# Kernel optimization log

Measured on AMD Instinct MI355X. Metric: run time of the kernel, lower is better.

## Reference

```python
import jax, jax.numpy as jnp
import numpy as np

NEG_SLOPE = 0.2
STRONG_CONVEXITY = 0.5


def _scalar(x, Wq, Wl, bl, Wz, wz_out, wq_out, wl_out):
    # x: [B, D]; Wq/Wl: [L, H, D]; bl: [L, H]; Wz: [L-1, H, H]
    # Precompute all per-layer x-dependent terms in two batched einsums.
    qx = jnp.einsum('lhd,bd->lbh', Wq, x) ** 2          # [L, B, H]
    lx = jnp.einsum('lhd,bd->lbh', Wl, x) + bl[:, None, :]  # [L, B, H]
    z = jax.nn.leaky_relu(qx[0] + lx[0], negative_slope=NEG_SLOPE)

    def step(z, inputs):
        W, q, l = inputs
        z = jax.nn.leaky_relu(z @ W.T + q + l, negative_slope=NEG_SLOPE)
        return z, None

    z, _ = jax.lax.scan(step, z, (Wz, qx[1:], lx[1:]))
    # Final layer to scalar output (no bias on last wx_lin per torch code).
    out = z @ wz_out.T + (x @ wq_out.T) ** 2 + x @ wl_out.T  # [B, 1]
    return out


def setup_inputs() -> dict:
    key = jax.random.key(0)
    ks = jax.random.split(key, 8)
    B, D, H, L = 8192, 128, 512, 10
    f32 = jnp.float32
    x = jax.random.normal(ks[0], (B, D), f32)
    Wq = jax.random.normal(ks[1], (L, H, D), f32) * (1.0 / np.sqrt(D))
    Wl = jax.random.normal(ks[2], (L, H, D), f32) * (1.0 / np.sqrt(D))
    bl = jax.random.normal(ks[3], (L, H), f32) * 0.01
    # wz weights are kept non-negative in the original (clamp/exp init)
    Wz = jnp.abs(jax.random.normal(ks[4], (L - 1, H, H), f32)) * (1.0 / np.sqrt(H))
    wz_out = jnp.abs(jax.random.normal(ks[5], (1, H), f32)) * (1.0 / np.sqrt(H))
    wq_out = jax.random.normal(ks[6], (1, D), f32) * (1.0 / np.sqrt(D))
    wl_out = jax.random.normal(ks[7], (1, D), f32) * (1.0 / np.sqrt(D))
    return {"x": x, "Wq": Wq, "Wl": Wl, "bl": bl, "Wz": Wz,
            "wz_out": wz_out, "wq_out": wq_out, "wl_out": wl_out}


def reference(x, Wq, Wl, bl, Wz, wz_out, wq_out, wl_out):
    # forward = (1 - mu) * d(scalar)/dx + mu * x, with grad_outputs = ones
    def scalar_sum(xx):
        return jnp.sum(_scalar(xx, Wq, Wl, bl, Wz, wz_out, wq_out, wl_out))

    gx = jax.grad(scalar_sum)(x)  # per-sample gradient, [B, D]
    return (1.0 - STRONG_CONVEXITY) * gx + STRONG_CONVEXITY * x
```

## Files before the change

### kernel.cpp

```cpp
#include <hip/hip_runtime.h>


#define Bn 8192
#define Dn 128
#define Hn 512
#define Ln 10

constexpr float NS = 0.2f;

typedef __attribute__((ext_vector_type(8))) short short8;
typedef __attribute__((ext_vector_type(4))) float f32x4;

typedef const __attribute__((address_space(1))) void GV;
typedef __attribute__((address_space(3))) void LV;

__device__ __forceinline__ void gload16(const void* g, void* l) {
    __builtin_amdgcn_global_load_lds((GV*)g, (LV*)l, 16, 0, 0);
}

#define MFMA(acc, a, b) acc = __builtin_amdgcn_mfma_f32_16x16x32_bf16(a, b, acc, 0, 0, 0)

__device__ __forceinline__ unsigned short bf16_rne(float v) {
    unsigned u = __float_as_uint(v);
    u += 0x7FFFu + ((u >> 16) & 1u);
    return (unsigned short)(u >> 16);
}
__device__ __forceinline__ float bf2f(unsigned short h) {
    return __uint_as_float(((unsigned)h) << 16);
}
__device__ __forceinline__ void split2(float v, unsigned short& h, unsigned short& l) {
    h = bf16_rne(v);
    l = bf16_rne(v - bf2f(h));
}


__global__ __launch_bounds__(256) void split_flat(const float* __restrict__ in,
        unsigned short* __restrict__ hi, unsigned short* __restrict__ lo, int n4) {
    int i = blockIdx.x * 256 + threadIdx.x;
    if (i >= n4) return;
    float4 v = ((const float4*)in)[i];
    ushort4 h, l;
    split2(v.x, h.x, l.x);
    split2(v.y, h.y, l.y);
    split2(v.z, h.z, l.z);
    split2(v.w, h.w, l.w);
    ((ushort4*)hi)[i] = h;
    ((ushort4*)lo)[i] = l;
}

__global__ __launch_bounds__(256) void split_both(const float* __restrict__ in,
        unsigned short* __restrict__ hi, unsigned short* __restrict__ lo,
        unsigned short* __restrict__ thi, unsigned short* __restrict__ tlo,
        int R, int C) {
    __shared__ float t[32][33];
    const size_t off = (size_t)blockIdx.z * R * C;
    const float* src = in + off;
    unsigned short* sh_ = hi + off;
    unsigned short* sl_ = lo + off;
    unsigned short* dh = thi + off;
    unsigned short* dl = tlo + off;
    const int r0 = blockIdx.x * 32, c0 = blockIdx.y * 32;
    const int tr = threadIdx.x >> 5, tc = threadIdx.x & 31;
#pragma unroll
    for (int i = 0; i < 4; ++i) {
        size_t si = (size_t)(r0 + tr + 8 * i) * C + c0 + tc;
        float v = src[si];
        t[tr + 8 * i][tc] = v;
        unsigned short h, l; split2(v, h, l);
        sh_[si] = h; sl_[si] = l;
    }
    __syncthreads();
#pragma unroll
    for (int i = 0; i < 4; ++i) {
        float v = t[tc][tr + 8 * i];
        unsigned short h, l; split2(v, h, l);
        size_t o = (size_t)(c0 + tr + 8 * i) * R + r0 + tc;
        dh[o] = h; dl[o] = l;
    }
}


__global__ __launch_bounds__(256) void fwd_mfma(
    const unsigned short* __restrict__ xh, const unsigned short* __restrict__ xl,
    const unsigned short* __restrict__ zph, const unsigned short* __restrict__ zpl,
    const unsigned short* __restrict__ Wzh, const unsigned short* __restrict__ Wzl,
    const unsigned short* __restrict__ Wqh, const unsigned short* __restrict__ Wql,
    const unsigned short* __restrict__ Wlh, const unsigned short* __restrict__ Wll,
    const float* __restrict__ bl,
    unsigned short* __restrict__ zoh, unsigned short* __restrict__ zol,
    unsigned short* __restrict__ mask16,
    unsigned short* __restrict__ uoh, unsigned short* __restrict__ uol, int hasZ)
{
    __shared__ __align__(16) char smem[32768];
    unsigned short* Ah  = (unsigned short*)smem;
    unsigned short* Al  = (unsigned short*)(smem + 8192);
    unsigned short* B0h = (unsigned short*)(smem + 16384);
    unsigned short* B0l = (unsigned short*)(smem + 20480);
    unsigned short* B1h = (unsigned short*)(smem + 24576);
    unsigned short* B1l = (unsigned short*)(smem + 28672);

    const int tid = threadIdx.x;
    const int w = tid >> 6, lane = tid & 63;
    const int lq = lane >> 4, lc = lane & 15;
    const int wm = (w & 1) * 64, wn = (w >> 1) * 32;
    const int row0 = blockIdx.x * 128, col0 = blockIdx.y * 64;
    const int sr = lane >> 2, sk = (lane & 3) * 8;

    f32x4 accz[4][2], accu[4][2], accv[4][2];
#pragma unroll
    for (int i = 0; i < 4; ++i)
#pragma unroll
        for (int j = 0; j < 2; ++j)
#pragma unroll
            for (int r = 0; r < 4; ++r) { accz[i][j][r] = 0.f; accu[i][j][r] = 0.f; accv[i][j][r] = 0.f; }

    if (hasZ) {
        for (int k0 = 0; k0 < Hn; k0 += 32) {
            __syncthreads();
            for (int c = w; c < 8; c += 4) {
                size_t go = (size_t)(row0 + c * 16 + sr) * Hn + k0 + sk;
                gload16(zph + go, Ah + c * 512);
                gload16(zpl + go, Al + c * 512);
            }
            {
                int c = w;
                size_t go = (size_t)(col0 + c * 16 + sr) * Hn + k0 + sk;
                gload16(Wzh + go, B0h + c * 512);
                gload16(Wzl + go, B0l + c * 512);
            }
            __syncthreads();
            short8 ah[4], al[4];
#pragma unroll
            for (int mt = 0; mt < 4; ++mt) {
                int ao = (wm + mt * 16 + lc) * 32 + lq * 8;
                ah[mt] = *(const short8*)(Ah + ao);
                al[mt] = *(const short8*)(Al + ao);
            }
#pragma unroll
            for (int nt = 0; nt < 2; ++nt) {
                int bo = (wn + nt * 16 + lc) * 32 + lq * 8;
                short8 bh = *(const short8*)(B0h + bo);
                short8 bv = *(const short8*)(B0l + bo);
#pragma unroll
                for (int mt = 0; mt < 4; ++mt) {
                    MFMA(accz[mt][nt], ah[mt], bh);
                    MFMA(accz[mt][nt], ah[mt], bv);
                    MFMA(accz[mt][nt], al[mt], bh);
                }
            }
        }
    }

    for (int k0 = 0; k0 < Dn; k0 += 32) {
        __syncthreads();
        for (int c = w; c < 8; c += 4) {
            size_t go = (size_t)(row0 + c * 16 + sr) * Dn + k0 + sk;
            gload16(xh + go, Ah + c * 512);
            gload16(xl + go, Al + c * 512);
        }
        {
            int c = w;
            size_t go = (size_t)(col0 + c * 16 + sr) * Dn + k0 + sk;
            gload16(Wqh + go, B0h + c * 512);
            gload16(Wql + go, B0l + c * 512);
            gload16(Wlh + go, B1h + c * 512);
            gload16(Wll + go, B1l + c * 512);
        }
        __syncthreads();
        short8 ah[4], al[4];
#pragma unroll
        for (int mt = 0; mt < 4; ++mt) {
            int ao = (wm + mt * 16 + lc) * 32 + lq * 8;
            ah[mt] = *(const short8*)(Ah + ao);
            al[mt] = *(const short8*)(Al + ao);
        }
#pragma unroll
        for (int nt = 0; nt < 2; ++nt) {
            int bo = (wn + nt * 16 + lc) * 32 + lq * 8;
            short8 bqh = *(const short8*)(B0h + bo);
            short8 bql = *(const short8*)(B0l + bo);
            short8 blh = *(const short8*)(B1h + bo);
            short8 bll = *(const short8*)(B1l + bo);
#pragma unroll
            for (int mt = 0; mt < 4; ++mt) {
                MFMA(accu[mt][nt], ah[mt], bqh);
                MFMA(accu[mt][nt], ah[mt], bql);
                MFMA(accu[mt][nt], al[mt], bqh);
                MFMA(accv[mt][nt], ah[mt], blh);
                MFMA(accv[mt][nt], ah[mt], bll);
                MFMA(accv[mt][nt], al[mt], blh);
            }
        }
    }

#pragma unroll
    for (int nt = 0; nt < 2; ++nt) {
        const int colb = col0 + wn + nt * 16;
        const int col = colb + lc;
        const float blv = bl[col];
#pragma unroll
        for (int mt = 0; mt < 4; ++mt) {
            const int rowb = row0 + wm + mt * 16;
#pragma unroll
            for (int r = 0; r < 4; ++r) {
                float uq = accu[mt][nt][r];
                float pre = accz[mt][nt][r] + uq * uq + accv[mt][nt][r] + blv;
                bool m = pre >= 0.f;
                unsigned long long bal = __ballot(m);
                if (lc == 0) {
                    int rw = rowb + lq * 4 + r;
                    mask16[(size_t)rw * 32 + (colb >> 4)] =
                        (unsigned short)((bal >> (lq * 16)) & 0xFFFFull);
                }
                float zv = m ? pre : NS * pre;
                unsigned short h, l; split2(zv, h, l);
                size_t o = (size_t)(rowb + lq * 4 + r) * Hn + col;
                zoh[o] = h; zol[o] = l;
                unsigned short uhh, ull; split2(uq, uhh, ull);
                uoh[o] = uhh; uol[o] = ull;
            }
        }
    }
}


__global__ __launch_bounds__(256) void bwd_combo(
    const unsigned short* __restrict__ gah, const unsigned short* __restrict__ gal,
    const unsigned short* __restrict__ WzTh, const unsigned short* __restrict__ WzTl,
    const unsigned short* __restrict__ maskprev,
    unsigned short* __restrict__ goh, unsigned short* __restrict__ gol,
    unsigned short* uph, unsigned short* upl,
    const unsigned short* __restrict__ a1h_, const unsigned short* __restrict__ a1l_,
    const unsigned short* __restrict__ WqTh, const unsigned short* __restrict__ WqTl,
    const unsigned short* __restrict__ WlTh, const unsigned short* __restrict__ WlTl,
    float* __restrict__ gx, int addTo, int nG, int finalF,
    const float* __restrict__ xin, const float* __restrict__ s,
    const float* __restrict__ wq_out, const float* __restrict__ wl_out)
{
    __shared__ __align__(16) char smem[24576];
    const int bid = blockIdx.x;
    const int tid = threadIdx.x;
    const int w = tid >> 6, lane = tid & 63;
    const int lq = lane >> 4, lc = lane & 15;
    const int sr = lane >> 2, sk = (lane & 3) * 8;

    if (bid < nG) {
        unsigned short* Ah  = (unsigned short*)smem;
        unsigned short* Al  = (unsigned short*)(smem + 8192);
        unsigned short* B0h = (unsigned short*)(smem + 16384);
        unsigned short* B0l = (unsigned short*)(smem + 20480);
        const int wm = (w & 1) * 64, wn = (w >> 1) * 32;
        const int row0 = (bid & 63) * 128, col0 = (bid >> 6) * 64;

        f32x4 acc[4][2];
#pragma unroll
        for (int i = 0; i < 4; ++i)
#pragma unroll
            for (int j = 0; j < 2; ++j)
#pragma unroll
                for (int r = 0; r < 4; ++r) acc[i][j][r] = 0.f;

        for (int k0 = 0; k0 < Hn; k0 += 32) {
            __syncthreads();
            for (int c = w; c < 8; c += 4) {
                size_t go = (size_t)(row0 + c * 16 + sr) * Hn + k0 + sk;
                gload16(gah + go, Ah + c * 512);
                gload16(gal + go, Al + c * 512);
            }
            {
                int c = w;
                size_t go = (size_t)(col0 + c * 16 + sr) * Hn + k0 + sk;
                gload16(WzTh + go, B0h + c * 512);
                gload16(WzTl + go, B0l + c * 512);
            }
            __syncthreads();
            short8 ah[4], al[4];
#pragma unroll
            for (int mt = 0; mt < 4; ++mt) {
                int ao = (wm + mt * 16 + lc) * 32 + lq * 8;
                ah[mt] = *(const short8*)(Ah + ao);
                al[mt] = *(const short8*)(Al + ao);
            }
#pragma unroll
            for (int nt = 0; nt < 2; ++nt) {
                int bo = (wn + nt * 16 + lc) * 32 + lq * 8;
                short8 bh = *(const short8*)(B0h + bo);
                short8 bv = *(const short8*)(B0l + bo);
#pragma unroll
                for (int mt = 0; mt < 4; ++mt) {
                    MFMA(acc[mt][nt], ah[mt], bh);
                    MFMA(acc[mt][nt], ah[mt], bv);
                    MFMA(acc[mt][nt], al[mt], bh);
                }
            }
        }

#pragma unroll
        for (int nt = 0; nt < 2; ++nt) {
            const int colb = col0 + wn + nt * 16;
            const int col = colb + lc;
#pragma unroll
            for (int mt = 0; mt < 4; ++mt) {
                const int rowb = row0 + wm + mt * 16;
#pragma unroll
                for (int r = 0; r < 4; ++r) {
                    int row = rowb + lq * 4 + r;
                    unsigned short wbits = maskprev[(size_t)row * 32 + (colb >> 4)];
                    float f = ((wbits >> lc) & 1) ? 1.f : NS;
                    float v = acc[mt][nt][r] * f;
                    unsigned short h, l; split2(v, h, l);
                    size_t o = (size_t)row * Hn + col;
                    goh[o] = h; gol[o] = l;
                    float uv = bf2f(uph[o]) + bf2f(upl[o]);
                    float a1v = 2.f * uv * v;
                    unsigned short h2, l2; split2(a1v, h2, l2);
                    uph[o] = h2; upl[o] = l2;
                }
            }
        }
    } else {
        unsigned short* Ah = (unsigned short*)smem;
        unsigned short* Al = (unsigned short*)(smem + 4096);
        unsigned short* Bh = (unsigned short*)(smem + 8192);
        unsigned short* Bl = (unsigned short*)(smem + 12288);
        const int wm = (w & 1) * 32, wn = (w >> 1) * 32;
        const int t = bid - nG;
        const int row0 = (t >> 1) * 64, col0 = (t & 1) * 64;

        f32x4 acc[2][2];
#pragma unroll
        for (int i = 0; i < 2; ++i)
#pragma unroll
            for (int j = 0; j < 2; ++j)
#pragma unroll
                for (int r = 0; r < 4; ++r) acc[i][j][r] = 0.f;

#pragma unroll
        for (int pass = 0; pass < 2; ++pass) {
            const unsigned short* Ash = pass ? gah : a1h_;
            const unsigned short* Asl = pass ? gal : a1l_;
            const unsigned short* Bsh = pass ? WlTh : WqTh;
            const unsigned short* Bsl = pass ? WlTl : WqTl;
            for (int k0 = 0; k0 < Hn; k0 += 32) {
                __syncthreads();
                {
                    int c = w;
                    size_t ga_ = (size_t)(row0 + c * 16 + sr) * Hn + k0 + sk;
                    gload16(Ash + ga_, Ah + c * 512);
                    gload16(Asl + ga_, Al + c * 512);
                    size_t gb_ = (size_t)(col0 + c * 16 + sr) * Hn + k0 + sk;
                    gload16(Bsh + gb_, Bh + c * 512);
                    gload16(Bsl + gb_, Bl + c * 512);
                }
                __syncthreads();
                short8 ah[2], al[2];
#pragma unroll
                for (int mt = 0; mt < 2; ++mt) {
                    int ao = (wm + mt * 16 + lc) * 32 + lq * 8;
                    ah[mt] = *(const short8*)(Ah + ao);
                    al[mt] = *(const short8*)(Al + ao);
                }
#pragma unroll
                for (int nt = 0; nt < 2; ++nt) {
                    int bo = (wn + nt * 16 + lc) * 32 + lq * 8;
                    short8 bh = *(const short8*)(Bh + bo);
                    short8 bv = *(const short8*)(Bl + bo);
#pragma unroll
                    for (int mt = 0; mt < 2; ++mt) {
                        MFMA(acc[mt][nt], ah[mt], bh);
                        MFMA(acc[mt][nt], ah[mt], bv);
                        MFMA(acc[mt][nt], al[mt], bh);
                    }
                }
            }
        }

#pragma unroll
        for (int nt = 0; nt < 2; ++nt) {
            const int col = col0 + wn + nt * 16 + lc;
#pragma unroll
            for (int mt = 0; mt < 2; ++mt) {
                const int rowb = row0 + wm + mt * 16;
#pragma unroll
                for (int r = 0; r < 4; ++r) {
                    const int row = rowb + lq * 4 + r;
                    size_t o = (size_t)row * Dn + col;
                    float v = acc[mt][nt][r];
                    if (addTo) v += gx[o];
                    if (finalF) {
                        v = 0.5f * v + s[row] * wq_out[col] + 0.5f * wl_out[col]
                            + 0.5f * xin[o];
                    }
                    gx[o] = v;
                }
            }
        }
    }
}


__global__ __launch_bounds__(256) void ga_init(
    const float* __restrict__ wz_out, const unsigned short* __restrict__ mask9,
    unsigned short* uh, unsigned short* ul,
    unsigned short* __restrict__ gh, unsigned short* __restrict__ gl)
{
    int i = blockIdx.x * 256 + threadIdx.x;
    int e = i << 2;
    int b = e >> 9, h = e & 511;
    unsigned short wbits = mask9[(size_t)b * 32 + (h >> 4)];
    float4 wv = *(const float4*)(wz_out + h);
    ushort4 u4h = *(const ushort4*)(uh + e);
    ushort4 u4l = *(const ushort4*)(ul + e);
    int sh = h & 15;
    ushort4 oh, ol, qh, ql;
    float f, a;
    f = wv.x * (((wbits >> (sh + 0)) & 1) ? 1.f : NS); split2(f, oh.x, ol.x);
    a = 2.f * (bf2f(u4h.x) + bf2f(u4l.x)) * f; split2(a, qh.x, ql.x);
    f = wv.y * (((wbits >> (sh + 1)) & 1) ? 1.f : NS); split2(f, oh.y, ol.y);
    a = 2.f * (bf2f(u4h.y) + bf2f(u4l.y)) * f; split2(a, qh.y, ql.y);
    f = wv.z * (((wbits >> (sh + 2)) & 1) ? 1.f : NS); split2(f, oh.z, ol.z);
    a = 2.f * (bf2f(u4h.z) + bf2f(u4l.z)) * f; split2(a, qh.z, ql.z);
    f = wv.w * (((wbits >> (sh + 3)) & 1) ? 1.f : NS); split2(f, oh.w, ol.w);
    a = 2.f * (bf2f(u4h.w) + bf2f(u4l.w)) * f; split2(a, qh.w, ql.w);
    *(ushort4*)(gh + e) = oh;
    *(ushort4*)(gl + e) = ol;
    *(ushort4*)(uh + e) = qh;
    *(ushort4*)(ul + e) = ql;
}

__global__ __launch_bounds__(256) void rowdot_kernel(
    const float* __restrict__ x, const float* __restrict__ wq_out, float* __restrict__ s) {
    const int b = blockIdx.x * 4 + (threadIdx.x >> 6);
    const int lane = threadIdx.x & 63;
    float v = x[(size_t)b * Dn + lane] * wq_out[lane] +
              x[(size_t)b * Dn + 64 + lane] * wq_out[64 + lane];
#pragma unroll
    for (int off = 32; off > 0; off >>= 1) v += __shfl_down(v, off, 64);
    if (lane == 0) s[b] = v;
}


extern "C" void kernel_launch(void* const* d_in, const int* in_sizes, int n_in,
                              void* d_out, int out_size, void* d_ws, size_t ws_size,
                              hipStream_t stream) {
    (void)in_sizes; (void)n_in; (void)out_size; (void)ws_size;
    const float* x      = (const float*)d_in[0];
    const float* Wq     = (const float*)d_in[1];
    const float* Wl     = (const float*)d_in[2];
    const float* bl     = (const float*)d_in[3];
    const float* Wz     = (const float*)d_in[4];
    const float* wz_out = (const float*)d_in[5];
    const float* wq_out = (const float*)d_in[6];
    const float* wl_out = (const float*)d_in[7];
    float* out = (float*)d_out;

    char* p = (char*)d_ws;
    #define CARVE(name, bytes) unsigned short* name = (unsigned short*)p; p += (((size_t)(bytes)) + 255) & ~(size_t)255;
    CARVE(xh,  (size_t)Bn*Dn*2)  CARVE(xl,  (size_t)Bn*Dn*2)
    CARVE(Wqh, (size_t)Ln*Hn*Dn*2) CARVE(Wql, (size_t)Ln*Hn*Dn*2)
    CARVE(Wlh, (size_t)Ln*Hn*Dn*2) CARVE(Wll, (size_t)Ln*Hn*Dn*2)
    CARVE(WqTh,(size_t)Ln*Hn*Dn*2) CARVE(WqTl,(size_t)Ln*Hn*Dn*2)
    CARVE(WlTh,(size_t)Ln*Hn*Dn*2) CARVE(WlTl,(size_t)Ln*Hn*Dn*2)
    CARVE(Wzh, (size_t)(Ln-1)*Hn*Hn*2) CARVE(Wzl, (size_t)(Ln-1)*Hn*Hn*2)
    CARVE(WzTh,(size_t)(Ln-1)*Hn*Hn*2) CARVE(WzTl,(size_t)(Ln-1)*Hn*Hn*2)
    CARVE(zAh, (size_t)Bn*Hn*2) CARVE(zAl, (size_t)Bn*Hn*2)
    CARVE(zBh, (size_t)Bn*Hn*2) CARVE(zBl, (size_t)Bn*Hn*2)
    CARVE(uLh, (size_t)Ln*Bn*Hn*2) CARVE(uLl, (size_t)Ln*Bn*Hn*2)
    float* s = (float*)p; p += (size_t)Bn*4;
    unsigned short* mask16 = (unsigned short*)p; p += (size_t)Ln*Bn*32*2;
    #undef CARVE

    split_flat<<<(Bn*Dn/4 + 255)/256, 256, 0, stream>>>(x, xh, xl, Bn*Dn/4);
    split_both<<<dim3(Hn/32, Dn/32, Ln), 256, 0, stream>>>(Wq, Wqh, Wql, WqTh, WqTl, Hn, Dn);
    split_both<<<dim3(Hn/32, Dn/32, Ln), 256, 0, stream>>>(Wl, Wlh, Wll, WlTh, WlTl, Hn, Dn);
    split_both<<<dim3(Hn/32, Hn/32, Ln-1), 256, 0, stream>>>(Wz, Wzh, Wzl, WzTh, WzTl, Hn, Hn);

    rowdot_kernel<<<Bn/4, 256, 0, stream>>>(x, wq_out, s);

    const dim3 gF(Bn/128, Hn/64);

    fwd_mfma<<<gF, 256, 0, stream>>>(xh, xl, nullptr, nullptr, nullptr, nullptr,
        Wqh, Wql, Wlh, Wll, bl, zAh, zAl, mask16, uLh, uLl, 0);
    for (int l = 1; l < Ln; ++l) {
        const unsigned short* zh  = (l & 1) ? zAh : zBh;
        const unsigned short* zl_ = (l & 1) ? zAl : zBl;
        unsigned short* oh  = (l & 1) ? zBh : zAh;
        unsigned short* ol_ = (l & 1) ? zBl : zAl;
        fwd_mfma<<<gF, 256, 0, stream>>>(xh, xl, zh, zl_,
            Wzh + (size_t)(l-1)*Hn*Hn, Wzl + (size_t)(l-1)*Hn*Hn,
            Wqh + (size_t)l*Hn*Dn, Wql + (size_t)l*Hn*Dn,
            Wlh + (size_t)l*Hn*Dn, Wll + (size_t)l*Hn*Dn,
            bl + (size_t)l*Hn, oh, ol_, mask16 + (size_t)l*Bn*32,
            uLh + (size_t)l*Bn*Hn, uLl + (size_t)l*Bn*Hn, 1);
    }

    ga_init<<<(Bn*Hn/4)/256, 256, 0, stream>>>(wz_out, mask16 + (size_t)9*Bn*32,
        uLh + (size_t)9*Bn*Hn, uLl + (size_t)9*Bn*Hn, zAh, zAl);
    for (int l = Ln - 1; l >= 0; --l) {
        int sidx = (Ln - 1 - l) & 1;
        const unsigned short* gh_  = sidx ? zBh : zAh;
        const unsigned short* gl_  = sidx ? zBl : zAl;
        unsigned short* oh   = sidx ? zAh : zBh;
        unsigned short* ol_  = sidx ? zAl : zBl;
        const int nG = (l > 0) ? 512 : 0;
        bwd_combo<<<nG + 256, 256, 0, stream>>>(
            gh_, gl_,
            (l > 0) ? WzTh + (size_t)(l-1)*Hn*Hn : nullptr,
            (l > 0) ? WzTl + (size_t)(l-1)*Hn*Hn : nullptr,
            (l > 0) ? mask16 + (size_t)(l-1)*Bn*32 : nullptr,
            (l > 0) ? oh : nullptr, (l > 0) ? ol_ : nullptr,
            (l > 0) ? uLh + (size_t)(l-1)*Bn*Hn : nullptr,
            (l > 0) ? uLl + (size_t)(l-1)*Bn*Hn : nullptr,
            uLh + (size_t)l*Bn*Hn, uLl + (size_t)l*Bn*Hn,
            WqTh + (size_t)l*Dn*Hn, WqTl + (size_t)l*Dn*Hn,
            WlTh + (size_t)l*Dn*Hn, WlTl + (size_t)l*Dn*Hn,
            out, (l == Ln - 1) ? 0 : 1, nG, (l == 0) ? 1 : 0,
            x, s, wq_out, wl_out);
    }
}
```

Baseline: 868.3 us.

## Double-buffer LDS loads and enlarge backward GEMM tile in bwd_combo

Both branches of the backward combo kernel now use double-buffered shared-memory staging, so the next K-slice is loaded asynchronously while MFMAs run on the current one, with one barrier per iteration instead of two. The Wz-gradient branch tile grows from 128x64 to 128x128, halving its block count and doubling B-operand reuse per A load. Shared memory rises to 64KB per block, which lowers occupancy, and register use grows with the 4x4 accumulator array.

```diff
diff --git a/kernel.cpp b/kernel.cpp
--- a/kernel.cpp
+++ b/kernel.cpp
@@ -237,7 +237,7 @@
     const float* __restrict__ xin, const float* __restrict__ s,
     const float* __restrict__ wq_out, const float* __restrict__ wl_out)
 {
-    __shared__ __align__(16) char smem[24576];
+    __shared__ __align__(16) char smem[65536];
     const int bid = blockIdx.x;
     const int tid = threadIdx.x;
     const int w = tid >> 6, lane = tid & 63;
@@ -245,35 +245,43 @@
     const int sr = lane >> 2, sk = (lane & 3) * 8;
 
     if (bid < nG) {
-        unsigned short* Ah  = (unsigned short*)smem;
-        unsigned short* Al  = (unsigned short*)(smem + 8192);
-        unsigned short* B0h = (unsigned short*)(smem + 16384);
-        unsigned short* B0l = (unsigned short*)(smem + 20480);
-        const int wm = (w & 1) * 64, wn = (w >> 1) * 32;
-        const int row0 = (bid & 63) * 128, col0 = (bid >> 6) * 64;
-
-        f32x4 acc[4][2];
+        const int wm = (w & 1) * 64, wn = (w >> 1) * 64;
+        const int row0 = (bid & 63) * 128, col0 = (bid >> 6) * 128;
+
+        f32x4 acc[4][4];
 #pragma unroll
         for (int i = 0; i < 4; ++i)
 #pragma unroll
-            for (int j = 0; j < 2; ++j)
+            for (int j = 0; j < 4; ++j)
 #pragma unroll
                 for (int r = 0; r < 4; ++r) acc[i][j][r] = 0.f;
 
-        for (int k0 = 0; k0 < Hn; k0 += 32) {
-            __syncthreads();
+        auto STAGE = [&](int buf, int k0) {
+            char* base = smem + buf * 32768;
+            unsigned short* Ah = (unsigned short*)base;
+            unsigned short* Al = (unsigned short*)(base + 8192);
+            unsigned short* Bh = (unsigned short*)(base + 16384);
+            unsigned short* Bl = (unsigned short*)(base + 24576);
             for (int c = w; c < 8; c += 4) {
                 size_t go = (size_t)(row0 + c * 16 + sr) * Hn + k0 + sk;
                 gload16(gah + go, Ah + c * 512);
                 gload16(gal + go, Al + c * 512);
-            }
-            {
-                int c = w;
-                size_t go = (size_t)(col0 + c * 16 + sr) * Hn + k0 + sk;
-                gload16(WzTh + go, B0h + c * 512);
-                gload16(WzTl + go, B0l + c * 512);
-            }
-            __syncthreads();
+                size_t gb = (size_t)(col0 + c * 16 + sr) * Hn + k0 + sk;
+                gload16(WzTh + gb, Bh + c * 512);
+                gload16(WzTl + gb, Bl + c * 512);
+            }
+        };
+
+        STAGE(0, 0);
+        __syncthreads();
+        int cur = 0;
+        for (int it = 0; it < 16; ++it) {
+            if (it < 15) STAGE(cur ^ 1, (it + 1) * 32);
+            const char* base = smem + cur * 32768;
+            const unsigned short* Ah = (const unsigned short*)base;
+            const unsigned short* Al = (const unsigned short*)(base + 8192);
+            const unsigned short* Bh = (const unsigned short*)(base + 16384);
+            const unsigned short* Bl = (const unsigned short*)(base + 24576);
             short8 ah[4], al[4];
 #pragma unroll
             for (int mt = 0; mt < 4; ++mt) {
@@ -282,10 +290,10 @@
                 al[mt] = *(const short8*)(Al + ao);
             }
 #pragma unroll
-            for (int nt = 0; nt < 2; ++nt) {
+            for (int nt = 0; nt < 4; ++nt) {
                 int bo = (wn + nt * 16 + lc) * 32 + lq * 8;
-                short8 bh = *(const short8*)(B0h + bo);
-                short8 bv = *(const short8*)(B0l + bo);
+                short8 bh = *(const short8*)(Bh + bo);
+                short8 bv = *(const short8*)(Bl + bo);
 #pragma unroll
                 for (int mt = 0; mt < 4; ++mt) {
                     MFMA(acc[mt][nt], ah[mt], bh);
@@ -293,10 +301,11 @@
                     MFMA(acc[mt][nt], al[mt], bh);
                 }
             }
-        }
-
-#pragma unroll
-        for (int nt = 0; nt < 2; ++nt) {
+            if (it < 15) { __syncthreads(); cur ^= 1; }
+        }
+
+#pragma unroll
+        for (int nt = 0; nt < 4; ++nt) {
             const int colb = col0 + wn + nt * 16;
             const int col = colb + lc;
 #pragma unroll
@@ -319,10 +328,6 @@
             }
         }
     } else {
-        unsigned short* Ah = (unsigned short*)smem;
-        unsigned short* Al = (unsigned short*)(smem + 4096);
-        unsigned short* Bh = (unsigned short*)(smem + 8192);
-        unsigned short* Bl = (unsigned short*)(smem + 12288);
         const int wm = (w & 1) * 32, wn = (w >> 1) * 32;
         const int t = bid - nG;
         const int row0 = (t >> 1) * 64, col0 = (t & 1) * 64;
@@ -335,44 +340,56 @@
 #pragma unroll
                 for (int r = 0; r < 4; ++r) acc[i][j][r] = 0.f;
 
-#pragma unroll
-        for (int pass = 0; pass < 2; ++pass) {
+        auto STAGE = [&](int buf, int j) {
+            int pass = j >> 4, k0 = (j & 15) * 32;
             const unsigned short* Ash = pass ? gah : a1h_;
             const unsigned short* Asl = pass ? gal : a1l_;
             const unsigned short* Bsh = pass ? WlTh : WqTh;
             const unsigned short* Bsl = pass ? WlTl : WqTl;
-            for (int k0 = 0; k0 < Hn; k0 += 32) {
-                __syncthreads();
-                {
-                    int c = w;
-                    size_t ga_ = (size_t)(row0 + c * 16 + sr) * Hn + k0 + sk;
-                    gload16(Ash + ga_, Ah + c * 512);
-                    gload16(Asl + ga_, Al + c * 512);
-                    size_t gb_ = (size_t)(col0 + c * 16 + sr) * Hn + k0 + sk;
-                    gload16(Bsh + gb_, Bh + c * 512);
-                    gload16(Bsl + gb_, Bl + c * 512);
+            char* base = smem + buf * 16384;
+            unsigned short* Ah = (unsigned short*)base;
+            unsigned short* Al = (unsigned short*)(base + 4096);
+            unsigned short* Bh = (unsigned short*)(base + 8192);
+            unsigned short* Bl = (unsigned short*)(base + 12288);
+            int c = w;
+            size_t ga_ = (size_t)(row0 + c * 16 + sr) * Hn + k0 + sk;
+            gload16(Ash + ga_, Ah + c * 512);
+            gload16(Asl + ga_, Al + c * 512);
+            size_t gb_ = (size_t)(col0 + c * 16 + sr) * Hn + k0 + sk;
+            gload16(Bsh + gb_, Bh + c * 512);
+            gload16(Bsl + gb_, Bl + c * 512);
+        };
+
+        STAGE(0, 0);
+        __syncthreads();
+        int cur = 0;
+        for (int j = 0; j < 32; ++j) {
+            if (j < 31) STAGE(cur ^ 1, j + 1);
+            const char* base = smem + cur * 16384;
+            const unsigned short* Ah = (const unsigned short*)base;
+            const unsigned short* Al = (const unsigned short*)(base + 4096);
+            const unsigned short* Bh = (const unsigned short*)(base + 8192);
+            const unsigned short* Bl = (const unsigned short*)(base + 12288);
+            short8 ah[2], al[2];
+#pragma unroll
+            for (int mt = 0; mt < 2; ++mt) {
+                int ao = (wm + mt * 16 + lc) * 32 + lq * 8;
+                ah[mt] = *(const short8*)(Ah + ao);
+                al[mt] = *(const short8*)(Al + ao);
+            }
+#pragma unroll
+            for (int nt = 0; nt < 2; ++nt) {
+                int bo = (wn + nt * 16 + lc) * 32 + lq * 8;
+                short8 bh = *(const short8*)(Bh + bo);
+                short8 bv = *(const short8*)(Bl + bo);
+#pragma unroll
+                for (int mt = 0; mt < 2; ++mt) {
+                    MFMA(acc[mt][nt], ah[mt], bh);
+                    MFMA(acc[mt][nt], ah[mt], bv);
+                    MFMA(acc[mt][nt], al[mt], bh);
                 }
-                __syncthreads();
-                short8 ah[2], al[2];
-#pragma unroll
-                for (int mt = 0; mt < 2; ++mt) {
-                    int ao = (wm + mt * 16 + lc) * 32 + lq * 8;
-                    ah[mt] = *(const short8*)(Ah + ao);
-                    al[mt] = *(const short8*)(Al + ao);
-                }
-#pragma unroll
-                for (int nt = 0; nt < 2; ++nt) {
-                    int bo = (wn + nt * 16 + lc) * 32 + lq * 8;
-                    short8 bh = *(const short8*)(Bh + bo);
-                    short8 bv = *(const short8*)(Bl + bo);
-#pragma unroll
-                    for (int mt = 0; mt < 2; ++mt) {
-                        MFMA(acc[mt][nt], ah[mt], bh);
-                        MFMA(acc[mt][nt], ah[mt], bv);
-                        MFMA(acc[mt][nt], al[mt], bh);
-                    }
-                }
-            }
+            }
+            if (j < 31) { __syncthreads(); cur ^= 1; }
         }
 
 #pragma unroll
@@ -502,7 +519,7 @@
         const unsigned short* gl_  = sidx ? zBl : zAl;
         unsigned short* oh   = sidx ? zAh : zBh;
         unsigned short* ol_  = sidx ? zAl : zBl;
-        const int nG = (l > 0) ? 512 : 0;
+        const int nG = (l > 0) ? 256 : 0;
         bwd_combo<<<nG + 256, 256, 0, stream>>>(
             gh_, gl_,
             (l > 0) ? WzTh + (size_t)(l-1)*Hn*Hn : nullptr,
```

After: 1.099 ms. +26.6%, slower.
